# Kernel optimization log

Measured on AMD Instinct MI355X. Metric: run time of the kernel, lower is better.

The kernel has to match this reference:

```python
import jax, jax.numpy as jnp
import numpy as np

B, LQ, LK, D = 8, 2048, 2048, 1024


def setup_inputs() -> dict:
    key = jax.random.key(0)
    k1, k2, k3, k4, k5 = jax.random.split(key, 5)
    inp = jax.random.normal(k1, (B, LQ, D), dtype=jnp.float32)
    memory = jax.random.normal(k2, (B, LK, D), dtype=jnp.float32)
    # 0/1 float mask over memory positions (1 = masked out)
    mask = (jax.random.uniform(k3, (B, LK)) < 0.15).astype(jnp.float32)
    # nn.Linear(D, 1, bias=False): weight shape [1, D], kaiming-uniform-ish init
    w_input = jax.random.uniform(k4, (1, D), dtype=jnp.float32,
                                 minval=-1.0 / np.sqrt(D), maxval=1.0 / np.sqrt(D))
    # dot_scale ~ U(0, 1/sqrt(D)) per original .uniform_(1/input_size**0.5)
    dot_scale = jax.random.uniform(k5, (D,), dtype=jnp.float32,
                                   minval=0.0, maxval=1.0 / np.sqrt(D))
    return {"input": inp, "memory": memory, "mask": mask,
            "w_input": w_input, "dot_scale": dot_scale}


def reference(input, memory, mask, w_input, dot_scale):
    # input_dot: Linear(D,1,bias=False) -> [B, Lq, 1]
    input_dot = jnp.einsum('bqd,od->bqo', input, w_input)  # o == 1
    # cross_dot: (input * dot_scale) @ memory^T -> [B, Lq, Lk]
    cross_dot = jnp.einsum('bqd,bkd->bqk', input * dot_scale, memory)
    att = input_dot + cross_dot - 1e30 * mask[:, None, :]
    weight_one = jax.nn.softmax(att, axis=-1)  # [B, Lq, Lk]
    output_one = jnp.einsum('bqk,bkd->bqd', weight_one, memory)
    return output_one
```

## Files before the change

kernel.cpp:

```cpp
#include <hip/hip_runtime.h>

#define B_  8
#define LQ_ 2048
#define LK_ 2048
#define D_  1024

typedef unsigned short u16;
using short8  = __attribute__((ext_vector_type(8))) short;
using floatx4 = __attribute__((ext_vector_type(4))) float;

#define GAS __attribute__((address_space(1)))
#define LAS __attribute__((address_space(3)))

__device__ __forceinline__ u16 f2bf(float f) {
  unsigned u = __float_as_uint(f);
  u += 0x7fffu + ((u >> 16) & 1u);
  return (u16)(u >> 16);
}
__device__ __forceinline__ float bf2f(u16 h) {
  return __uint_as_float(((unsigned)h) << 16);
}

__global__ void prep(const float* __restrict__ in, const float* __restrict__ mem,
                     const float* __restrict__ ds, u16* __restrict__ qb,
                     u16* __restrict__ mb, u16* __restrict__ mbT,
                     float* __restrict__ denom) {
  __shared__ u16 tile[64][68];
  int tid = threadIdx.x;
  int tx = tid & 15, ty = tid >> 4;
  int b = blockIdx.z;

  if (denom && blockIdx.y == 16 && blockIdx.x == 0 && blockIdx.z == 0) {
    float4 z = {0.f, 0.f, 0.f, 0.f};
    float4* d4 = (float4*)denom;
#pragma unroll
    for (int i = 0; i < (B_ * LQ_ / 4) / 256; i++)
      d4[tid + i * 256] = z;
  }

  if (blockIdx.y < 16) {
    int k0 = blockIdx.x * 64, d0 = blockIdx.y * 64;
    const float* mB = mem + (size_t)b * LK_ * D_;
    u16* mbB = mb  + (size_t)b * LK_ * D_;
    u16* mtB = mbT + (size_t)b * D_ * LK_;
#pragma unroll
    for (int i = 0; i < 4; i++) {
      int r = ty + 16 * i;
      float4 v = *(const float4*)(mB + (size_t)(k0 + r) * D_ + d0 + tx * 4);
      ushort4 h;
      h.x = f2bf(v.x); h.y = f2bf(v.y); h.z = f2bf(v.z); h.w = f2bf(v.w);
      *(ushort4*)(mbB + (size_t)(k0 + r) * D_ + d0 + tx * 4) = h;
      *(ushort4*)(&tile[r][tx * 4]) = h;
    }
    __syncthreads();
#pragma unroll
    for (int i = 0; i < 4; i++) {
      int rr = ty + 16 * i;
      ushort4 o;
      o.x = tile[tx * 4 + 0][rr];
      o.y = tile[tx * 4 + 1][rr];
      o.z = tile[tx * 4 + 2][rr];
      o.w = tile[tx * 4 + 3][rr];
      *(ushort4*)(mtB + (size_t)(d0 + rr) * LK_ + k0 + tx * 4) = o;
    }
  } else {
    int q0 = blockIdx.x * 64, d0 = (blockIdx.y - 16) * 64;
    const float* iB = in + (size_t)b * LQ_ * D_;
    u16* qB = qb + (size_t)b * LQ_ * D_;
    float4 s4 = *(const float4*)(ds + d0 + tx * 4);
#pragma unroll
    for (int i = 0; i < 4; i++) {
      int r = ty + 16 * i;
      float4 v = *(const float4*)(iB + (size_t)(q0 + r) * D_ + d0 + tx * 4);
      ushort4 h;
      h.x = f2bf(v.x * s4.x); h.y = f2bf(v.y * s4.y);
      h.z = f2bf(v.z * s4.z); h.w = f2bf(v.w * s4.w);
      *(ushort4*)(qB + (size_t)(q0 + r) * D_ + d0 + tx * 4) = h;
    }
  }
}

template <int MODE>
__global__ __launch_bounds__(512, 2) void gemm_bt(
    const u16* __restrict__ A, const u16* __restrict__ Bm,
    void* __restrict__ C, const float* __restrict__ mask,
    float* __restrict__ denom, int K, int ld, int ldc,
    size_t sA, size_t sB, size_t sC) {
  __shared__ __align__(16) u16 As[4 * 8192];
  __shared__ __align__(16) u16 Bs[4 * 8192];

  const int tid = threadIdx.x;
  const int lane = tid & 63, w = tid >> 6;
  const int lm = lane & 15, quad = (lane >> 4) & 3;
  const int wm = (w >> 2) * 128, wn = (w & 3) * 64;

  const int tiles_n = gridDim.x;
  int bid = (blockIdx.z * gridDim.y + blockIdx.y) * tiles_n + blockIdx.x;
  int bz = bid & 7;
  int s = bid >> 3;
  const int GM = 4;
  int per_group = GM * tiles_n;
  int group = s / per_group;
  int rem = s - group * per_group;
  int tm = group * GM + (rem & (GM - 1));
  int tn = rem >> 2;

  const u16* Ab = A  + (size_t)bz * sA + (size_t)(tm * 256) * ld;
  const u16* Bb = Bm + (size_t)bz * sB + (size_t)(tn * 256) * ld;

  int goff[2], ldst[2];
#pragma unroll
  for (int j = 0; j < 2; j++) {
    int c = tid + 512 * j;
    int row = c >> 2;
    int slot = (c & 3) ^ ((row >> 1) & 3);
    goff[j] = row * ld + slot * 8;
    ldst[j] = c * 8;
  }

  const int sw = quad ^ ((lm >> 1) & 3);
  const int aoff = (wm + lm) * 32 + sw * 8;
  const int boff = (wn + lm) * 32 + sw * 8;

  auto stageA = [&](int koff, int plane) {
#pragma unroll
    for (int j = 0; j < 2; j++)
      __builtin_amdgcn_global_load_lds((GAS void*)(Ab + goff[j] + koff),
                                       (LAS void*)(As + (plane << 13) + ldst[j]),
                                       16, 0, 0);
  };
  auto stageB = [&](int koff, int plane) {
#pragma unroll
    for (int j = 0; j < 2; j++)
      __builtin_amdgcn_global_load_lds((GAS void*)(Bb + goff[j] + koff),
                                       (LAS void*)(Bs + (plane << 13) + ldst[j]),
                                       16, 0, 0);
  };

  floatx4 acc[8][4];
#pragma unroll
  for (int i = 0; i < 8; i++)
#pragma unroll
    for (int j = 0; j < 4; j++)
      acc[i][j] = {0.f, 0.f, 0.f, 0.f};

  float rs[8] = {0.f, 0.f, 0.f, 0.f, 0.f, 0.f, 0.f, 0.f};

#define WAIT4 { asm volatile("s_waitcnt vmcnt(4)" ::: "memory"); \
                __builtin_amdgcn_sched_barrier(0); }
#define WAIT0 { asm volatile("s_waitcnt vmcnt(0)" ::: "memory"); \
                __builtin_amdgcn_sched_barrier(0); }

#define PHASE(KK, CUR, STG, W)                                                \
  {                                                                           \
    __builtin_amdgcn_sched_barrier(0);                                        \
    const u16* Ap = As + (((CUR) * 2 + (KK)) << 13);                          \
    const u16* Bp = Bs + (((CUR) * 2 + (KK)) << 13);                          \
    short8 bf[4], af[8];                                                      \
    _Pragma("unroll")                                                         \
    for (int n = 0; n < 4; n++)                                               \
      bf[n] = *(const short8*)(Bp + boff + n * 512);                          \
    _Pragma("unroll")                                                         \
    for (int m = 0; m < 8; m++)                                               \
      af[m] = *(const short8*)(Ap + aoff + m * 512);                          \
    STG;                                                                      \
    asm volatile("s_waitcnt lgkmcnt(8)" ::: "memory");                        \
    __builtin_amdgcn_sched_barrier(0);                                        \
    W;                                                                        \
    __builtin_amdgcn_s_barrier();                                             \
    asm volatile("s_waitcnt lgkmcnt(0)" ::: "memory");                        \
    __builtin_amdgcn_sched_barrier(0);                                        \
    if constexpr (MODE == 2) {                                                \
      _Pragma("unroll")                                                       \
      for (int m = 0; m < 8; m++) {                                           \
        uint4 u = *(const uint4*)&af[m];                                      \
        rs[m] +=                                                              \
            __uint_as_float(u.x << 16) + __uint_as_float(u.x & 0xffff0000u)   \
          + __uint_as_float(u.y << 16) + __uint_as_float(u.y & 0xffff0000u)   \
          + __uint_as_float(u.z << 16) + __uint_as_float(u.z & 0xffff0000u)   \
          + __uint_as_float(u.w << 16) + __uint_as_float(u.w & 0xffff0000u);  \
      }                                                                       \
    }                                                                         \
    __builtin_amdgcn_s_setprio(1);                                            \
    _Pragma("unroll")                                                         \
    for (int m = 0; m < 8; m++)                                               \
      _Pragma("unroll")                                                       \
      for (int n = 0; n < 4; n++)                                             \
        acc[m][n] = __builtin_amdgcn_mfma_f32_16x16x32_bf16(                  \
            af[m], bf[n], acc[m][n], 0, 0, 0);                                \
    __builtin_amdgcn_s_setprio(0);                                            \
    __builtin_amdgcn_sched_barrier(0);                                        \
  }

  const int NT = K >> 6;
  stageA(0, 0); stageB(0, 0); stageA(32, 1); stageB(32, 1);
  WAIT4;
  __builtin_amdgcn_s_barrier();

  for (int t = 0; t < NT; ++t) {
    const int cur = t & 1, nb = cur ^ 1;
    const bool have = (t + 1 < NT);
    const int k0n = (t + 1) << 6;

    PHASE(0, cur,
          if (have) { stageA(k0n, nb * 2); stageB(k0n, nb * 2); },
          if (have) WAIT4 else WAIT0)
    PHASE(1, cur,
          if (have) { stageA(k0n + 32, nb * 2 + 1); stageB(k0n + 32, nb * 2 + 1); },
          if (have) WAIT4)
  }
#undef PHASE
#undef WAIT4
#undef WAIT0

  const int gm0 = tm * 256 + wm + quad * 4;
  const int gn0 = tn * 256 + wn + lm;
  const size_t cb = (size_t)bz * sC;

  if constexpr (MODE == 1) {
    const float* mrow = mask + (size_t)bz * LK_;
    bool msk[4];
#pragma unroll
    for (int ni = 0; ni < 4; ni++) msk[ni] = (mrow[gn0 + ni * 16] != 0.0f);
#pragma unroll
    for (int mi = 0; mi < 8; mi++) {
#pragma unroll
      for (int r = 0; r < 4; r++) {
        int row = gm0 + mi * 16 + r;
        size_t rowoff = cb + (size_t)row * ldc + gn0;
        float part = 0.f;
#pragma unroll
        for (int ni = 0; ni < 4; ni++) {
          float e = msk[ni] ? 0.f : __expf(acc[mi][ni][r]);
          u16 h = f2bf(e);
          ((u16*)C)[rowoff + ni * 16] = h;
          part += bf2f(h);
        }
        if (denom) {
          part += __shfl_xor(part, 1, 64);
          part += __shfl_xor(part, 2, 64);
          part += __shfl_xor(part, 4, 64);
          part += __shfl_xor(part, 8, 64);
          if (lm == 0) atomicAdd(&denom[(size_t)bz * LQ_ + row], part);
        }
      }
    }
  } else if constexpr (MODE == 0) {
#pragma unroll
    for (int mi = 0; mi < 8; mi++) {
#pragma unroll
      for (int r = 0; r < 4; r++) {
        int row = gm0 + mi * 16 + r;
        float is = 1.0f / denom[(size_t)bz * LQ_ + row];
        size_t rowoff = cb + (size_t)row * ldc + gn0;
#pragma unroll
        for (int ni = 0; ni < 4; ni++)
          ((float*)C)[rowoff + ni * 16] = acc[mi][ni][r] * is;
      }
    }
  } else {
    float inv[8];
#pragma unroll
    for (int mi = 0; mi < 8; mi++) {
      rs[mi] += __shfl_xor(rs[mi], 16, 64);
      rs[mi] += __shfl_xor(rs[mi], 32, 64);
      inv[mi] = 1.0f / rs[mi];
    }
#pragma unroll
    for (int mi = 0; mi < 8; mi++) {
#pragma unroll
      for (int r = 0; r < 4; r++) {
        size_t rowoff = cb + (size_t)(gm0 + mi * 16 + r) * ldc + gn0;
        float is = __shfl(inv[mi], quad * 4 + r, 64);
#pragma unroll
        for (int ni = 0; ni < 4; ni++)
          ((float*)C)[rowoff + ni * 16] = acc[mi][ni][r] * is;
      }
    }
  }
}

extern "C" void kernel_launch(void* const* d_in, const int* in_sizes, int n_in,
                              void* d_out, int out_size, void* d_ws, size_t ws_size,
                              hipStream_t stream) {
  const float* input  = (const float*)d_in[0];
  const float* memory = (const float*)d_in[1];
  const float* mask   = (const float*)d_in[2];
  const float* dscale = (const float*)d_in[4];

  char* ws = (char*)d_ws;
  u16* qb  = (u16*)(ws);
  u16* mb  = (u16*)(ws + (size_t)32 * 1024 * 1024);
  u16* mbT = (u16*)(ws + (size_t)64 * 1024 * 1024);
  u16* E   = (u16*)(ws + (size_t)96 * 1024 * 1024);
  size_t base = (size_t)160 * 1024 * 1024;
  bool have_denom = ws_size >= base + (size_t)B_ * LQ_ * sizeof(float);
  float* denom = have_denom ? (float*)(ws + base) : nullptr;
  float* out = (float*)d_out;

  hipLaunchKernelGGL(prep, dim3(32, 32, B_), dim3(256), 0, stream,
                     input, memory, dscale, qb, mb, mbT, denom);
  hipLaunchKernelGGL((gemm_bt<1>), dim3(LK_ / 256, LQ_ / 256, B_), dim3(512), 0,
                     stream, qb, mb, (void*)E, mask, denom, D_, D_, LK_,
                     (size_t)LQ_ * D_, (size_t)LK_ * D_, (size_t)LQ_ * LK_);
  if (have_denom)
    hipLaunchKernelGGL((gemm_bt<0>), dim3(D_ / 256, LQ_ / 256, B_), dim3(512), 0,
                       stream, E, mbT, (void*)out, nullptr, denom, LK_, LK_, D_,
                       (size_t)LQ_ * LK_, (size_t)D_ * LK_, (size_t)LQ_ * D_);
  else
    hipLaunchKernelGGL((gemm_bt<2>), dim3(D_ / 256, LQ_ / 256, B_), dim3(512), 0,
                       stream, E, mbT, (void*)out, nullptr, nullptr, LK_, LK_, D_,
                       (size_t)LQ_ * LK_, (size_t)D_ * LK_, (size_t)LQ_ * D_);
}
```

Baseline: 314.1 us.

## Restructure GEMM main loop into four sub-phases with register-bank ping-pong prefetch

Reworks the bf16 MFMA GEMM mainloop so each 64-wide K tile is split into four quadrant phases (A-half by B-half). LDS fragment reads for the next phase are issued ahead of the current phase's MFMAs using alternating register banks, and the global-to-LDS staging is split into smaller per-group loads spread across the phases. The LDS layout also changes from two 32-wide K planes to a single 64-wide row with an XOR swizzle. The goal is to hide LDS read latency behind MFMA work and smooth out the memory traffic. The cost is roughly double the fragment registers, which may hurt occupancy under launch_bounds(512,2), and more complex wait-count bookkeeping that is easy to get wrong.

```diff
diff --git a/kernel.cpp b/kernel.cpp
--- a/kernel.cpp
+++ b/kernel.cpp
@@ -86,8 +86,8 @@
     void* __restrict__ C, const float* __restrict__ mask,
     float* __restrict__ denom, int K, int ld, int ldc,
     size_t sA, size_t sB, size_t sC) {
-  __shared__ __align__(16) u16 As[4 * 8192];
-  __shared__ __align__(16) u16 Bs[4 * 8192];
+  __shared__ __align__(16) u16 As[2 * 16384];
+  __shared__ __align__(16) u16 Bs[2 * 16384];
 
   const int tid = threadIdx.x;
   const int lane = tid & 63, w = tid >> 6;
@@ -108,110 +108,137 @@
   const u16* Ab = A  + (size_t)bz * sA + (size_t)(tm * 256) * ld;
   const u16* Bb = Bm + (size_t)bz * sB + (size_t)(tn * 256) * ld;
 
-  int goff[2], ldst[2];
+  int goffA[2], ldsA[2], goffB[2], ldsB[2];
 #pragma unroll
   for (int j = 0; j < 2; j++) {
     int c = tid + 512 * j;
-    int row = c >> 2;
-    int slot = (c & 3) ^ ((row >> 1) & 3);
-    goff[j] = row * ld + slot * 8;
-    ldst[j] = c * 8;
-  }
-
-  const int sw = quad ^ ((lm >> 1) & 3);
-  const int aoff = (wm + lm) * 32 + sw * 8;
-  const int boff = (wn + lm) * 32 + sw * 8;
-
-  auto stageA = [&](int koff, int plane) {
+    int rho = c >> 3, sl = c & 7;
+    int rA = (rho & 63) + ((rho >> 6) << 7);
+    int rB = (rho & 31) + ((rho >> 5) << 6);
+    int gsl = (sl ^ (rho & 7)) * 8;
+    goffA[j] = rA * ld + gsl;
+    ldsA[j]  = rA * 64 + sl * 8;
+    goffB[j] = rB * ld + gsl;
+    ldsB[j]  = rB * 64 + sl * 8;
+  }
+
+  auto stA = [&](int g, int buf, int k0) {
 #pragma unroll
     for (int j = 0; j < 2; j++)
-      __builtin_amdgcn_global_load_lds((GAS void*)(Ab + goff[j] + koff),
-                                       (LAS void*)(As + (plane << 13) + ldst[j]),
-                                       16, 0, 0);
+      __builtin_amdgcn_global_load_lds(
+          (GAS void*)(Ab + (size_t)g * 64 * ld + goffA[j] + k0),
+          (LAS void*)(As + buf * 16384 + g * 4096 + ldsA[j]), 16, 0, 0);
   };
-  auto stageB = [&](int koff, int plane) {
+  auto stB = [&](int g, int buf, int k0) {
 #pragma unroll
     for (int j = 0; j < 2; j++)
-      __builtin_amdgcn_global_load_lds((GAS void*)(Bb + goff[j] + koff),
-                                       (LAS void*)(Bs + (plane << 13) + ldst[j]),
-                                       16, 0, 0);
+      __builtin_amdgcn_global_load_lds(
+          (GAS void*)(Bb + (size_t)g * 32 * ld + goffB[j] + k0),
+          (LAS void*)(Bs + buf * 16384 + g * 2048 + ldsB[j]), 16, 0, 0);
   };
 
+  const int ka0 = ((0 + quad) ^ (lm & 7)) * 8;
+  const int ka1 = ((4 + quad) ^ (lm & 7)) * 8;
+
+  short8 afA[8], afB[8], bfP[4], bfQ[4];
   floatx4 acc[8][4];
 #pragma unroll
   for (int i = 0; i < 8; i++)
 #pragma unroll
     for (int j = 0; j < 4; j++)
       acc[i][j] = {0.f, 0.f, 0.f, 0.f};
-
   float rs[8] = {0.f, 0.f, 0.f, 0.f, 0.f, 0.f, 0.f, 0.f};
 
-#define WAIT4 { asm volatile("s_waitcnt vmcnt(4)" ::: "memory"); \
+#define VW(N) { asm volatile("s_waitcnt vmcnt(" #N ")" ::: "memory"); \
                 __builtin_amdgcn_sched_barrier(0); }
-#define WAIT0 { asm volatile("s_waitcnt vmcnt(0)" ::: "memory"); \
-                __builtin_amdgcn_sched_barrier(0); }
-
-#define PHASE(KK, CUR, STG, W)                                                \
+
+#define RD_A(BANK, MH, BB)                                                    \
+  { _Pragma("unroll")                                                         \
+    for (int m = 0; m < 4; m++) {                                             \
+      BANK[m*2+0] = *(const short8*)(As + (BB)*16384 +                        \
+          ((wm + (MH)*64 + m*16 + lm) << 6) + ka0);                           \
+      BANK[m*2+1] = *(const short8*)(As + (BB)*16384 +                        \
+          ((wm + (MH)*64 + m*16 + lm) << 6) + ka1);                           \
+    } }
+#define RD_B(BANK, NH, BB)                                                    \
+  { _Pragma("unroll")                                                         \
+    for (int n = 0; n < 2; n++) {                                             \
+      BANK[n*2+0] = *(const short8*)(Bs + (BB)*16384 +                        \
+          ((wn + (NH)*32 + n*16 + lm) << 6) + ka0);                           \
+      BANK[n*2+1] = *(const short8*)(Bs + (BB)*16384 +                        \
+          ((wn + (NH)*32 + n*16 + lm) << 6) + ka1);                           \
+    } }
+#define SUMA(BANK, O)                                                         \
+  if constexpr (MODE == 2) {                                                  \
+    _Pragma("unroll")                                                         \
+    for (int m = 0; m < 8; m++) {                                             \
+      uint4 u = *(const uint4*)&BANK[m];                                      \
+      rs[(O) + (m >> 1)] +=                                                   \
+          __uint_as_float(u.x << 16) + __uint_as_float(u.x & 0xffff0000u)     \
+        + __uint_as_float(u.y << 16) + __uint_as_float(u.y & 0xffff0000u)     \
+        + __uint_as_float(u.z << 16) + __uint_as_float(u.z & 0xffff0000u)     \
+        + __uint_as_float(u.w << 16) + __uint_as_float(u.w & 0xffff0000u);    \
+    } }
+
+#define PH(STG, WAITS, SUMS, READS, MH, NH, ABANK, BBANK)                     \
   {                                                                           \
     __builtin_amdgcn_sched_barrier(0);                                        \
-    const u16* Ap = As + (((CUR) * 2 + (KK)) << 13);                          \
-    const u16* Bp = Bs + (((CUR) * 2 + (KK)) << 13);                          \
-    short8 bf[4], af[8];                                                      \
-    _Pragma("unroll")                                                         \
-    for (int n = 0; n < 4; n++)                                               \
-      bf[n] = *(const short8*)(Bp + boff + n * 512);                          \
-    _Pragma("unroll")                                                         \
-    for (int m = 0; m < 8; m++)                                               \
-      af[m] = *(const short8*)(Ap + aoff + m * 512);                          \
     STG;                                                                      \
-    asm volatile("s_waitcnt lgkmcnt(8)" ::: "memory");                        \
-    __builtin_amdgcn_sched_barrier(0);                                        \
-    W;                                                                        \
+    WAITS;                                                                    \
     __builtin_amdgcn_s_barrier();                                             \
     asm volatile("s_waitcnt lgkmcnt(0)" ::: "memory");                        \
     __builtin_amdgcn_sched_barrier(0);                                        \
-    if constexpr (MODE == 2) {                                                \
-      _Pragma("unroll")                                                       \
-      for (int m = 0; m < 8; m++) {                                           \
-        uint4 u = *(const uint4*)&af[m];                                      \
-        rs[m] +=                                                              \
-            __uint_as_float(u.x << 16) + __uint_as_float(u.x & 0xffff0000u)   \
-          + __uint_as_float(u.y << 16) + __uint_as_float(u.y & 0xffff0000u)   \
-          + __uint_as_float(u.z << 16) + __uint_as_float(u.z & 0xffff0000u)   \
-          + __uint_as_float(u.w << 16) + __uint_as_float(u.w & 0xffff0000u);  \
-      }                                                                       \
-    }                                                                         \
+    SUMS;                                                                     \
+    READS;                                                                    \
+    __builtin_amdgcn_sched_barrier(0);                                        \
     __builtin_amdgcn_s_setprio(1);                                            \
     _Pragma("unroll")                                                         \
-    for (int m = 0; m < 8; m++)                                               \
+    for (int m = 0; m < 4; m++)                                               \
       _Pragma("unroll")                                                       \
-      for (int n = 0; n < 4; n++)                                             \
-        acc[m][n] = __builtin_amdgcn_mfma_f32_16x16x32_bf16(                  \
-            af[m], bf[n], acc[m][n], 0, 0, 0);                                \
+      for (int n = 0; n < 2; n++)                                             \
+        _Pragma("unroll")                                                     \
+        for (int ks = 0; ks < 2; ks++)                                        \
+          acc[(MH)*4+m][(NH)*2+n] = __builtin_amdgcn_mfma_f32_16x16x32_bf16(  \
+              ABANK[m*2+ks], BBANK[n*2+ks], acc[(MH)*4+m][(NH)*2+n], 0,0,0);  \
     __builtin_amdgcn_s_setprio(0);                                            \
     __builtin_amdgcn_sched_barrier(0);                                        \
   }
 
+#define TILE(CUR, NB, BI, BO, HAVE, KN)                                       \
+  PH(if (HAVE) stA(0, NB, KN),                                                \
+     if (HAVE) { VW(4) } else { VW(2) },                                      \
+     SUMA(afA, 0),                                                            \
+     RD_B(BO, 1, CUR),                                                        \
+     0, 0, afA, BI)                                                           \
+  PH(if (HAVE) stB(0, NB, KN),                                                \
+     if (HAVE) { VW(4) } else { VW(0) },                                      \
+     {},                                                                      \
+     RD_A(afB, 1, CUR),                                                       \
+     0, 1, afA, BO)                                                           \
+  PH(if (HAVE) stB(1, NB, KN), {}, SUMA(afB, 4), {}, 1, 1, afB, BO)           \
+  PH(if (HAVE) stA(1, NB, KN),                                                \
+     if (HAVE) { VW(4) },                                                     \
+     {},                                                                      \
+     if (HAVE) { RD_A(afA, 0, NB) RD_B(BO, 0, NB) },                          \
+     1, 0, afB, BI)
+
   const int NT = K >> 6;
-  stageA(0, 0); stageB(0, 0); stageA(32, 1); stageB(32, 1);
-  WAIT4;
+  stA(0, 0, 0); stB(0, 0, 0); stB(1, 0, 0); stA(1, 0, 0);
+  VW(4);
   __builtin_amdgcn_s_barrier();
-
-  for (int t = 0; t < NT; ++t) {
-    const int cur = t & 1, nb = cur ^ 1;
-    const bool have = (t + 1 < NT);
-    const int k0n = (t + 1) << 6;
-
-    PHASE(0, cur,
-          if (have) { stageA(k0n, nb * 2); stageB(k0n, nb * 2); },
-          if (have) WAIT4 else WAIT0)
-    PHASE(1, cur,
-          if (have) { stageA(k0n + 32, nb * 2 + 1); stageB(k0n + 32, nb * 2 + 1); },
-          if (have) WAIT4)
-  }
-#undef PHASE
-#undef WAIT4
-#undef WAIT0
+  RD_A(afA, 0, 0)
+  RD_B(bfP, 0, 0)
+
+  for (int tt = 0; tt < NT; tt += 2) {
+    TILE(0, 1, bfP, bfQ, true, (tt + 1) << 6)
+    TILE(1, 0, bfQ, bfP, (tt + 2 < NT), (tt + 2) << 6)
+  }
+#undef TILE
+#undef PH
+#undef RD_A
+#undef RD_B
+#undef SUMA
+#undef VW
 
   const int gm0 = tm * 256 + wm + quad * 4;
   const int gn0 = tn * 256 + wn + lm;
```

Result: slower. 369.7 us (+17.7%).
